# Performance work log

Measured on AMD Instinct MI355X. Metric: run time of the kernel, lower is better.

Reference implementation:

```python
import jax, jax.numpy as jnp
import numpy as np

STATE_DIM = 512
MAX_STEPS = 16
BATCH = 4096
NOISE_SCALE = 0.1


def setup_inputs() -> dict:
    key = jax.random.key(0)
    ks = jax.random.split(key, 12)
    D = STATE_DIM
    init = lambda k, shape, scale: (jax.random.normal(k, shape, dtype=jnp.float32) * scale)
    inp = {
        'initial_state': init(ks[0], (BATCH, D), 1.0),
        'noise': init(ks[1], (MAX_STEPS, BATCH, D), 1.0),
        # initial_v_proj: Linear(D, D)
        'Wv': init(ks[2], (D, D), 0.02), 'bv': jnp.zeros((D,), jnp.float32),
        # evidence_transform: Linear(2D, D) -> tanh -> Linear(D, D)
        'W1': init(ks[3], (D, 2 * D), 0.02), 'b1': jnp.zeros((D,), jnp.float32),
        'W2': init(ks[4], (D, D), 0.02), 'b2': jnp.zeros((D,), jnp.float32),
        # noise_gate: Linear(1,32) -> ReLU -> Linear(32,1) -> Sigmoid
        'Wg1': init(ks[5], (32, 1), 0.5), 'bg1': jnp.zeros((32,), jnp.float32),
        'Wg2': init(ks[6], (1, 32), 0.5), 'bg2': jnp.zeros((1,), jnp.float32),
        # clamped scalar params
        'raw_decay': jnp.float32(0.9),
        'raw_dt': jnp.float32(0.1),
        'raw_spring': jnp.float32(0.5),
        'raw_threshold': jnp.float32(0.05),
    }
    return inp


def reference(initial_state, noise, Wv, bv, W1, b1, W2, b2, Wg1, bg1, Wg2, bg2,
              raw_decay, raw_dt, raw_spring, raw_threshold):
    decay = jnp.clip(raw_decay, 0.5, 0.99)
    dt = jnp.clip(raw_dt, 0.01, 0.5)
    spring = jnp.abs(raw_spring) + 0.01
    threshold = jnp.abs(raw_threshold) + 0.0001

    x0 = initial_state
    v0 = initial_state @ Wv.T + bv  # initial_v_proj

    def step(carry, noise_t):
        x, v = carry
        gz = jnp.linalg.norm(v, axis=-1, keepdims=True)  # (B,1)
        # hopfield is None -> retrieved = zeros_like(x)
        evidence_in = jnp.concatenate([x, jnp.zeros_like(x)], axis=-1)  # (B,2D)
        force = spring * (jnp.tanh(evidence_in @ W1.T + b1) @ W2.T + b2)
        gate = jax.nn.sigmoid(jax.nn.relu(gz @ Wg1.T + bg1) @ Wg2.T + bg2)  # (B,1)
        v_new = decay * v + force + noise_t * gate * NOISE_SCALE
        x_new = x + dt * v_new
        return (x_new, v_new), (x_new, v_new, jnp.mean(gz[:, 0]))

    (xf, vf), (xs, vs, gzs) = jax.lax.scan(step, (x0, v0), noise)
    positions = jnp.concatenate([x0[None], xs], axis=0)    # (17, B, D)
    velocities = jnp.concatenate([v0[None], vs], axis=0)   # (17, B, D)
    gray_zones = jnp.concatenate(
        [jnp.mean(jnp.linalg.norm(v0, axis=-1))[None], gzs], axis=0)  # (17,)
    converged = jnp.linalg.norm(vf, axis=-1) < jax.lax.stop_gradient(threshold)
    return xf, vf, positions, velocities, gray_zones, converged
```

## Files before the change

kernel.cpp:

```cpp
#include <hip/hip_runtime.h>
#include <hip/hip_bf16.h>

#define DIM      512
#define NSTEPS   16

#define OFF_XF   0
#define OFF_VF   2097152
#define OFF_POS  4194304
#define OFF_VEL  39845888
#define OFF_GZ   75497472
#define OFF_CONV 75497489
#define SLAB     2097152

#define WS_WV 0
#define WS_W1 524288
#define WS_W2 1048576
#define WS_GZ 1572864

typedef __attribute__((ext_vector_type(8))) short short8v;
typedef __attribute__((ext_vector_type(4))) float f32x4;

__device__ __forceinline__ unsigned short f2bf(float f) {
  union { float f; unsigned u; } a; a.f = f;
  return (unsigned short)((a.u + 0x7FFFu + ((a.u >> 16) & 1u)) >> 16);
}

__device__ __forceinline__ float tanh_fast(float x) {
  float e = __expf(2.0f * x);
  return 1.0f - 2.0f / (e + 1.0f);
}

__device__ __forceinline__ void st_bf(unsigned short* lds, int r, int c, float f) {
  int byte = (c << 1) ^ ((r & 7) << 4);
  *(unsigned short*)((char*)lds + (r << 10) + byte) = f2bf(f);
}

__global__ void prep_kernel(const float* __restrict__ Wv,
                            const float* __restrict__ W1,
                            const float* __restrict__ W2,
                            unsigned short* __restrict__ ws) {
  int t = blockIdx.x * 256 + threadIdx.x;
  if (t < 32) ((float*)(ws + WS_GZ / 2))[t] = 0.0f;
  int lane = t & 63, kt = (t >> 6) & 15, nt = (t >> 10) & 31, mat = t >> 15;
  const float* W = (mat == 0) ? Wv : (mat == 1) ? W1 : W2;
  int stride = (mat == 1) ? 1024 : 512;
  unsigned short* o = ws + (mat == 0 ? WS_WV / 2 : mat == 1 ? WS_W1 / 2 : WS_W2 / 2);
  int row = nt * 16 + (lane & 15);
  int col = kt * 32 + (lane >> 4) * 8;
  const float* src = W + row * stride + col;
  short8v v;
#pragma unroll
  for (int j = 0; j < 8; ++j) v[j] = (short)f2bf(src[j]);
  *(short8v*)(o + (((nt * 16 + kt) * 64 + lane) * 8)) = v;
}

#define GEMM_512(WB) do {                                                     \
    const short8v* __wv = (const short8v*)(WB);                               \
    _Pragma("unroll")                                                         \
    for (int nt_ = 0; nt_ < 8; ++nt_) acc[nt_] = (f32x4){0.f, 0.f, 0.f, 0.f};\
    _Pragma("unroll 2")                                                       \
    for (int kt_ = 0; kt_ < 16; ++kt_) {                                      \
      short8v a_ = *(const short8v*)(aptr + ((kt_ * 64 + acol0) ^ aswz));     \
      short8v b_[8];                                                          \
      _Pragma("unroll")                                                       \
      for (int nt_ = 0; nt_ < 8; ++nt_)                                       \
        b_[nt_] = __wv[((ng8 + nt_) * 16 + kt_) * 64 + lane];                 \
      _Pragma("unroll")                                                       \
      for (int nt_ = 0; nt_ < 8; ++nt_)                                       \
        acc[nt_] = __builtin_amdgcn_mfma_f32_16x16x32_bf16(a_, b_[nt_],       \
                                                           acc[nt_], 0, 0, 0);\
    }                                                                         \
  } while (0)

__launch_bounds__(512)
__global__ void main_kernel(const float* __restrict__ x0,
                            const float* __restrict__ noise,
                            const float* __restrict__ bv,
                            const float* __restrict__ b1,
                            const float* __restrict__ b2,
                            const float* __restrict__ Wg1,
                            const float* __restrict__ bg1,
                            const float* __restrict__ Wg2,
                            const float* __restrict__ bg2,
                            const float* __restrict__ rdecay,
                            const float* __restrict__ rdt,
                            const float* __restrict__ rspring,
                            const float* __restrict__ rthr,
                            const unsigned short* __restrict__ ws,
                            float* __restrict__ gzsum,
                            float* __restrict__ out) {
  __shared__ unsigned short a_lds[32 * 512];
  __shared__ float gz_p[32];
  __shared__ float gate_lds[32];

  const int tid  = threadIdx.x;
  const int lane = tid & 63;
  const int w    = tid >> 6;
  const int mt   = w & 1;
  const int ng   = w >> 1;
  const int ng8  = ng * 8;
  const int lg   = lane >> 4;
  const int li   = lane & 15;
  const int base = blockIdx.x * 32;

  const float decay  = fminf(fmaxf(rdecay[0], 0.5f), 0.99f);
  const float dt     = fminf(fmaxf(rdt[0], 0.01f), 0.5f);
  const float spring = fabsf(rspring[0]) + 0.01f;

  const char* aptr = (const char*)a_lds + (mt * 16 + li) * 1024;
  const int acol0 = lg * 16;
  const int aswz  = (li & 7) << 4;

  int colv[8], rowv[4], rg[4];
  float b1c[8], b2c[8], bvc[8];
#pragma unroll
  for (int nt = 0; nt < 8; ++nt) {
    colv[nt] = ng * 128 + nt * 16 + li;
    b1c[nt] = b1[colv[nt]]; b2c[nt] = b2[colv[nt]]; bvc[nt] = bv[colv[nt]];
  }
#pragma unroll
  for (int j = 0; j < 4; ++j) { rowv[j] = mt * 16 + lg * 4 + j; rg[j] = (base + rowv[j]) * DIM; }

  for (int i = tid; i < 32 * DIM; i += 512) {
    int r = i >> 9, c = i & 511;
    st_bf(a_lds, r, c, x0[(base + r) * DIM + c]);
  }
  float x[8][4], v[8][4];
#pragma unroll
  for (int nt = 0; nt < 8; ++nt)
#pragma unroll
    for (int j = 0; j < 4; ++j) x[nt][j] = x0[rg[j] + colv[nt]];
  __syncthreads();

  f32x4 acc[8];
  GEMM_512(ws + WS_WV / 2);
#pragma unroll
  for (int nt = 0; nt < 8; ++nt)
#pragma unroll
    for (int j = 0; j < 4; ++j) {
      v[nt][j] = acc[nt][j] + bvc[nt];
      out[OFF_VEL + rg[j] + colv[nt]] = v[nt][j];
    }

  for (int t = 0; t < NSTEPS; ++t) {
    __syncthreads();
    if (tid < 32) gz_p[tid] = 0.0f;
    if (t > 0) {
#pragma unroll
      for (int nt = 0; nt < 8; ++nt)
#pragma unroll
        for (int j = 0; j < 4; ++j) st_bf(a_lds, rowv[j], colv[nt], x[nt][j]);
    }
    __syncthreads();

#pragma unroll
    for (int j = 0; j < 4; ++j) {
      float s = 0.f;
#pragma unroll
      for (int nt = 0; nt < 8; ++nt) s += v[nt][j] * v[nt][j];
      s += __shfl_xor(s, 1); s += __shfl_xor(s, 2);
      s += __shfl_xor(s, 4); s += __shfl_xor(s, 8);
      if (li == 0) atomicAdd(&gz_p[rowv[j]], s);
    }
    __syncthreads();

    if (tid < 32) {
      float g = sqrtf(gz_p[tid]);
      float z = bg2[0];
#pragma unroll
      for (int k = 0; k < 32; ++k) {
        float a = fmaxf(fmaf(g, Wg1[k], bg1[k]), 0.0f);
        z = fmaf(Wg2[k], a, z);
      }
      gate_lds[tid] = 1.0f / (1.0f + __expf(-z));
      float bs = g;
      bs += __shfl_xor(bs, 1); bs += __shfl_xor(bs, 2); bs += __shfl_xor(bs, 4);
      bs += __shfl_xor(bs, 8); bs += __shfl_xor(bs, 16);
      if (tid == 0) {
        atomicAdd(&gzsum[t + 1], bs);
        if (t == 0) atomicAdd(&gzsum[0], bs);
      }
    }

    GEMM_512(ws + WS_W1 / 2);
    __syncthreads();
#pragma unroll
    for (int nt = 0; nt < 8; ++nt)
#pragma unroll
      for (int j = 0; j < 4; ++j)
        st_bf(a_lds, rowv[j], colv[nt], tanh_fast(acc[nt][j] + b1c[nt]));
    __syncthreads();

    float nz[8][4];
    const float* np = noise + (size_t)t * (4096 * DIM);
#pragma unroll
    for (int nt = 0; nt < 8; ++nt)
#pragma unroll
      for (int j = 0; j < 4; ++j) nz[nt][j] = np[rg[j] + colv[nt]];

    GEMM_512(ws + WS_W2 / 2);

    float* pos = out + OFF_POS + (size_t)(t + 1) * SLAB;
    float* vel = out + OFF_VEL + (size_t)(t + 1) * SLAB;
#pragma unroll
    for (int j = 0; j < 4; ++j) {
      float g = gate_lds[rowv[j]];
#pragma unroll
      for (int nt = 0; nt < 8; ++nt) {
        float force = spring * (acc[nt][j] + b2c[nt]);
        float vn = fmaf(decay, v[nt][j], force) + nz[nt][j] * g * 0.1f;
        v[nt][j] = vn;
        x[nt][j] = fmaf(dt, vn, x[nt][j]);
        int gi = rg[j] + colv[nt];
        pos[gi] = x[nt][j];
        vel[gi] = vn;
        if (t == NSTEPS - 1) { out[OFF_XF + gi] = x[nt][j]; out[OFF_VF + gi] = vn; }
      }
    }
  }

  if (tid < 32) gz_p[tid] = 0.0f;
  __syncthreads();
#pragma unroll
  for (int j = 0; j < 4; ++j) {
    float s = 0.f;
#pragma unroll
    for (int nt = 0; nt < 8; ++nt) s += v[nt][j] * v[nt][j];
    s += __shfl_xor(s, 1); s += __shfl_xor(s, 2);
    s += __shfl_xor(s, 4); s += __shfl_xor(s, 8);
    if (li == 0) atomicAdd(&gz_p[rowv[j]], s);
  }
  __syncthreads();
  if (tid < 32) {
    float thr = fabsf(rthr[0]) + 1e-4f;
    out[OFF_CONV + base + tid] = (sqrtf(gz_p[tid]) < thr) ? 1.0f : 0.0f;
  }
}

__global__ void finalize_kernel(const float* __restrict__ gzsum,
                                float* __restrict__ out) {
  int t = threadIdx.x;
  if (t < 17) out[OFF_GZ + t] = gzsum[t] * (1.0f / 4096.0f);
}

extern "C" void kernel_launch(void* const* d_in, const int* in_sizes, int n_in,
                              void* d_out, int out_size, void* d_ws, size_t ws_size,
                              hipStream_t stream) {
  const float* x0     = (const float*)d_in[0];
  const float* noise  = (const float*)d_in[1];
  const float* Wv     = (const float*)d_in[2];
  const float* bv     = (const float*)d_in[3];
  const float* W1     = (const float*)d_in[4];
  const float* b1     = (const float*)d_in[5];
  const float* W2     = (const float*)d_in[6];
  const float* b2     = (const float*)d_in[7];
  const float* Wg1    = (const float*)d_in[8];
  const float* bg1    = (const float*)d_in[9];
  const float* Wg2    = (const float*)d_in[10];
  const float* bg2    = (const float*)d_in[11];
  const float* rdec   = (const float*)d_in[12];
  const float* rdt    = (const float*)d_in[13];
  const float* rspr   = (const float*)d_in[14];
  const float* rthr   = (const float*)d_in[15];
  unsigned short* ws  = (unsigned short*)d_ws;
  float* gz           = (float*)((char*)d_ws + WS_GZ);
  float* out          = (float*)d_out;

  hipMemcpyAsync(out + OFF_POS, x0, (size_t)4096 * DIM * sizeof(float),
                 hipMemcpyDeviceToDevice, stream);
  prep_kernel<<<384, 256, 0, stream>>>(Wv, W1, W2, ws);
  main_kernel<<<128, 512, 0, stream>>>(x0, noise, bv, b1, b2, Wg1, bg1, Wg2, bg2,
                                       rdec, rdt, rspr, rthr, ws, gz, out);
  finalize_kernel<<<1, 32, 0, stream>>>(gz, out);
}
```

Before: 675.7 us.

## Split batch into 16-row blocks with 16 waves each, software-pipelined MFMA loads

Blocks now cover 16 rows instead of 32, launched as 256 blocks of 1024 threads, so all 256 CUs get work instead of half of them. Each wave computes a 16x32 output slice. The GEMM loop prefetches the next A and B fragments one k-step ahead. The step also drops one barrier, loads noise earlier, spreads the gate MLP across a full wave, and folds the x0-to-positions copy into the kernel in place of a separate memcpy. In exchange, each block reads the full weight matrices for only 16 rows, so weight traffic through L2 doubles, and the 1024-thread blocks limit registers per thread.

```diff
diff --git a/kernel.cpp b/kernel.cpp
--- a/kernel.cpp
+++ b/kernel.cpp
@@ -3,6 +3,7 @@
 
 #define DIM      512
 #define NSTEPS   16
+#define BATCH    4096
 
 #define OFF_XF   0
 #define OFF_VF   2097152
@@ -54,25 +55,26 @@
   *(short8v*)(o + (((nt * 16 + kt) * 64 + lane) * 8)) = v;
 }
 
-#define GEMM_512(WB) do {                                                     \
-    const short8v* __wv = (const short8v*)(WB);                               \
+#define LDA(kt)     (*(const short8v*)(aptr + ((((kt) * 64) + acol0) ^ aswz)))
+#define LDB(nt, kt) (wv[(((nt) * 16 + (kt)) * 64) + lane])
+
+#define GEMM_512(WBASE) do {                                                  \
+    const short8v* wv = (const short8v*)(WBASE) + (w * 2048);                 \
+    acc[0] = (f32x4){0.f, 0.f, 0.f, 0.f};                                     \
+    acc[1] = (f32x4){0.f, 0.f, 0.f, 0.f};                                     \
+    short8v aC = LDA(0), b0 = LDB(0, 0), b1 = LDB(1, 0);                      \
     _Pragma("unroll")                                                         \
-    for (int nt_ = 0; nt_ < 8; ++nt_) acc[nt_] = (f32x4){0.f, 0.f, 0.f, 0.f};\
-    _Pragma("unroll 2")                                                       \
     for (int kt_ = 0; kt_ < 16; ++kt_) {                                      \
-      short8v a_ = *(const short8v*)(aptr + ((kt_ * 64 + acol0) ^ aswz));     \
-      short8v b_[8];                                                          \
-      _Pragma("unroll")                                                       \
-      for (int nt_ = 0; nt_ < 8; ++nt_)                                       \
-        b_[nt_] = __wv[((ng8 + nt_) * 16 + kt_) * 64 + lane];                 \
-      _Pragma("unroll")                                                       \
-      for (int nt_ = 0; nt_ < 8; ++nt_)                                       \
-        acc[nt_] = __builtin_amdgcn_mfma_f32_16x16x32_bf16(a_, b_[nt_],       \
-                                                           acc[nt_], 0, 0, 0);\
+      short8v aN = aC, b0n = b0, b1n = b1;                                    \
+      if (kt_ < 15) { aN = LDA(kt_ + 1); b0n = LDB(0, kt_ + 1);               \
+                      b1n = LDB(1, kt_ + 1); }                                \
+      acc[0] = __builtin_amdgcn_mfma_f32_16x16x32_bf16(aC, b0, acc[0],0,0,0); \
+      acc[1] = __builtin_amdgcn_mfma_f32_16x16x32_bf16(aC, b1, acc[1],0,0,0); \
+      aC = aN; b0 = b0n; b1 = b1n;                                            \
     }                                                                         \
   } while (0)
 
-__launch_bounds__(512)
+__launch_bounds__(1024, 4)
 __global__ void main_kernel(const float* __restrict__ x0,
                             const float* __restrict__ noise,
                             const float* __restrict__ bv,
@@ -89,53 +91,54 @@
                             const unsigned short* __restrict__ ws,
                             float* __restrict__ gzsum,
                             float* __restrict__ out) {
-  __shared__ unsigned short a_lds[32 * 512];
-  __shared__ float gz_p[32];
-  __shared__ float gate_lds[32];
+  __shared__ unsigned short a_lds[16 * 512];
+  __shared__ float gz_p[16];
+  __shared__ float gate_lds[16];
 
   const int tid  = threadIdx.x;
   const int lane = tid & 63;
   const int w    = tid >> 6;
-  const int mt   = w & 1;
-  const int ng   = w >> 1;
-  const int ng8  = ng * 8;
   const int lg   = lane >> 4;
   const int li   = lane & 15;
-  const int base = blockIdx.x * 32;
+  const int base = blockIdx.x * 16;
 
   const float decay  = fminf(fmaxf(rdecay[0], 0.5f), 0.99f);
   const float dt     = fminf(fmaxf(rdt[0], 0.01f), 0.5f);
   const float spring = fabsf(rspring[0]) + 0.01f;
 
-  const char* aptr = (const char*)a_lds + (mt * 16 + li) * 1024;
+  const char* aptr = (const char*)a_lds + li * 1024;
   const int acol0 = lg * 16;
   const int aswz  = (li & 7) << 4;
 
-  int colv[8], rowv[4], rg[4];
-  float b1c[8], b2c[8], bvc[8];
-#pragma unroll
-  for (int nt = 0; nt < 8; ++nt) {
-    colv[nt] = ng * 128 + nt * 16 + li;
+  int colv[2], rowv[4], rg[4];
+  float b1c[2], b2c[2], bvc[2];
+#pragma unroll
+  for (int nt = 0; nt < 2; ++nt) {
+    colv[nt] = w * 32 + nt * 16 + li;
     b1c[nt] = b1[colv[nt]]; b2c[nt] = b2[colv[nt]]; bvc[nt] = bv[colv[nt]];
   }
 #pragma unroll
-  for (int j = 0; j < 4; ++j) { rowv[j] = mt * 16 + lg * 4 + j; rg[j] = (base + rowv[j]) * DIM; }
-
-  for (int i = tid; i < 32 * DIM; i += 512) {
-    int r = i >> 9, c = i & 511;
-    st_bf(a_lds, r, c, x0[(base + r) * DIM + c]);
-  }
-  float x[8][4], v[8][4];
-#pragma unroll
-  for (int nt = 0; nt < 8; ++nt)
+  for (int j = 0; j < 4; ++j) { rowv[j] = lg * 4 + j; rg[j] = (base + rowv[j]) * DIM; }
+
+  if (tid < 16) gz_p[tid] = 0.0f;
+  for (int i = tid; i < 16 * 128; i += 1024) {
+    int r = i >> 7, c4 = (i & 127) * 4;
+    const float4 xv = *(const float4*)&x0[(base + r) * DIM + c4];
+    st_bf(a_lds, r, c4 + 0, xv.x); st_bf(a_lds, r, c4 + 1, xv.y);
+    st_bf(a_lds, r, c4 + 2, xv.z); st_bf(a_lds, r, c4 + 3, xv.w);
+    *(float4*)&out[OFF_POS + (size_t)(base + r) * DIM + c4] = xv;
+  }
+  float x[2][4], v[2][4];
+#pragma unroll
+  for (int nt = 0; nt < 2; ++nt)
 #pragma unroll
     for (int j = 0; j < 4; ++j) x[nt][j] = x0[rg[j] + colv[nt]];
   __syncthreads();
 
-  f32x4 acc[8];
-  GEMM_512(ws + WS_WV / 2);
-#pragma unroll
-  for (int nt = 0; nt < 8; ++nt)
+  f32x4 acc[2];
+  GEMM_512((const short8v*)(ws + WS_WV / 2));
+#pragma unroll
+  for (int nt = 0; nt < 2; ++nt)
 #pragma unroll
     for (int j = 0; j < 4; ++j) {
       v[nt][j] = acc[nt][j] + bvc[nt];
@@ -144,69 +147,71 @@
 
   for (int t = 0; t < NSTEPS; ++t) {
     __syncthreads();
-    if (tid < 32) gz_p[tid] = 0.0f;
     if (t > 0) {
 #pragma unroll
-      for (int nt = 0; nt < 8; ++nt)
+      for (int nt = 0; nt < 2; ++nt)
 #pragma unroll
         for (int j = 0; j < 4; ++j) st_bf(a_lds, rowv[j], colv[nt], x[nt][j]);
     }
-    __syncthreads();
-
 #pragma unroll
     for (int j = 0; j < 4; ++j) {
       float s = 0.f;
 #pragma unroll
-      for (int nt = 0; nt < 8; ++nt) s += v[nt][j] * v[nt][j];
+      for (int nt = 0; nt < 2; ++nt) s += v[nt][j] * v[nt][j];
       s += __shfl_xor(s, 1); s += __shfl_xor(s, 2);
       s += __shfl_xor(s, 4); s += __shfl_xor(s, 8);
       if (li == 0) atomicAdd(&gz_p[rowv[j]], s);
     }
     __syncthreads();
 
-    if (tid < 32) {
-      float g = sqrtf(gz_p[tid]);
-      float z = bg2[0];
-#pragma unroll
-      for (int k = 0; k < 32; ++k) {
+    float nz[2][4];
+    {
+      const float* np = noise + (size_t)t * (BATCH * DIM);
+#pragma unroll
+      for (int nt = 0; nt < 2; ++nt)
+#pragma unroll
+        for (int j = 0; j < 4; ++j) nz[nt][j] = np[rg[j] + colv[nt]];
+    }
+    if (w == 0) {
+      int r = lane >> 2, p = lane & 3;
+      float g = sqrtf(gz_p[r]);
+      float z = 0.f;
+#pragma unroll
+      for (int kk = 0; kk < 8; ++kk) {
+        int k = p * 8 + kk;
         float a = fmaxf(fmaf(g, Wg1[k], bg1[k]), 0.0f);
         z = fmaf(Wg2[k], a, z);
       }
-      gate_lds[tid] = 1.0f / (1.0f + __expf(-z));
-      float bs = g;
-      bs += __shfl_xor(bs, 1); bs += __shfl_xor(bs, 2); bs += __shfl_xor(bs, 4);
-      bs += __shfl_xor(bs, 8); bs += __shfl_xor(bs, 16);
-      if (tid == 0) {
+      z += __shfl_xor(z, 1); z += __shfl_xor(z, 2);
+      if (p == 0) gate_lds[r] = 1.0f / (1.0f + __expf(-(z + bg2[0])));
+      float bs = (p == 0) ? g : 0.f;
+      bs += __shfl_xor(bs, 1);  bs += __shfl_xor(bs, 2);
+      bs += __shfl_xor(bs, 4);  bs += __shfl_xor(bs, 8);
+      bs += __shfl_xor(bs, 16); bs += __shfl_xor(bs, 32);
+      if (lane == 0) {
         atomicAdd(&gzsum[t + 1], bs);
         if (t == 0) atomicAdd(&gzsum[0], bs);
       }
     }
-
-    GEMM_512(ws + WS_W1 / 2);
-    __syncthreads();
-#pragma unroll
-    for (int nt = 0; nt < 8; ++nt)
+    GEMM_512((const short8v*)(ws + WS_W1 / 2));
+    __syncthreads();
+
+#pragma unroll
+    for (int nt = 0; nt < 2; ++nt)
 #pragma unroll
       for (int j = 0; j < 4; ++j)
         st_bf(a_lds, rowv[j], colv[nt], tanh_fast(acc[nt][j] + b1c[nt]));
-    __syncthreads();
-
-    float nz[8][4];
-    const float* np = noise + (size_t)t * (4096 * DIM);
-#pragma unroll
-    for (int nt = 0; nt < 8; ++nt)
-#pragma unroll
-      for (int j = 0; j < 4; ++j) nz[nt][j] = np[rg[j] + colv[nt]];
-
-    GEMM_512(ws + WS_W2 / 2);
-
+    if (tid < 16) gz_p[tid] = 0.0f;
+    __syncthreads();
+
+    GEMM_512((const short8v*)(ws + WS_W2 / 2));
     float* pos = out + OFF_POS + (size_t)(t + 1) * SLAB;
     float* vel = out + OFF_VEL + (size_t)(t + 1) * SLAB;
 #pragma unroll
     for (int j = 0; j < 4; ++j) {
       float g = gate_lds[rowv[j]];
 #pragma unroll
-      for (int nt = 0; nt < 8; ++nt) {
+      for (int nt = 0; nt < 2; ++nt) {
         float force = spring * (acc[nt][j] + b2c[nt]);
         float vn = fmaf(decay, v[nt][j], force) + nz[nt][j] * g * 0.1f;
         v[nt][j] = vn;
@@ -219,19 +224,17 @@
     }
   }
 
-  if (tid < 32) gz_p[tid] = 0.0f;
-  __syncthreads();
 #pragma unroll
   for (int j = 0; j < 4; ++j) {
     float s = 0.f;
 #pragma unroll
-    for (int nt = 0; nt < 8; ++nt) s += v[nt][j] * v[nt][j];
+    for (int nt = 0; nt < 2; ++nt) s += v[nt][j] * v[nt][j];
     s += __shfl_xor(s, 1); s += __shfl_xor(s, 2);
     s += __shfl_xor(s, 4); s += __shfl_xor(s, 8);
     if (li == 0) atomicAdd(&gz_p[rowv[j]], s);
   }
   __syncthreads();
-  if (tid < 32) {
+  if (tid < 16) {
     float thr = fabsf(rthr[0]) + 1e-4f;
     out[OFF_CONV + base + tid] = (sqrtf(gz_p[tid]) < thr) ? 1.0f : 0.0f;
   }
@@ -266,10 +269,8 @@
   float* gz           = (float*)((char*)d_ws + WS_GZ);
   float* out          = (float*)d_out;
 
-  hipMemcpyAsync(out + OFF_POS, x0, (size_t)4096 * DIM * sizeof(float),
-                 hipMemcpyDeviceToDevice, stream);
   prep_kernel<<<384, 256, 0, stream>>>(Wv, W1, W2, ws);
-  main_kernel<<<128, 512, 0, stream>>>(x0, noise, bv, b1, b2, Wg1, bg1, Wg2, bg2,
-                                       rdec, rdt, rspr, rthr, ws, gz, out);
+  main_kernel<<<256, 1024, 0, stream>>>(x0, noise, bv, b1, b2, Wg1, bg1, Wg2, bg2,
+                                        rdec, rdt, rspr, rthr, ws, gz, out);
   finalize_kernel<<<1, 32, 0, stream>>>(gz, out);
 }
```

Result: slower. 997.3 us (+47.6%).

## Double workgroup threads, software-pipeline GEMM loads, fuse x0 copy, use nontemporal stores

Applied to the files above, without the earlier changes.

Each 32-row block now runs 1024 threads (16 waves), so every wave covers 64 output columns with 4 accumulators instead of 128 with 8. The GEMM loop prefetches the next k-slice of A and B into registers while the current MFMAs issue. The separate device-to-device copy of x0 into positions is folded into the kernel's initial load, which is vectorised. Noise loads are issued earlier, before the first GEMM, and all outputs use nontemporal stores. Barriers are also reordered so the gz scratch is reset in a phase that already has a sync, which removes one barrier per step. The goal is more latency hiding and fewer launches and syncs, at the cost of more per-block synchronisation among 16 waves and register pressure under the 1024-thread launch bound.

```diff
diff --git a/kernel.cpp b/kernel.cpp
--- a/kernel.cpp
+++ b/kernel.cpp
@@ -3,6 +3,7 @@
 
 #define DIM      512
 #define NSTEPS   16
+#define BATCH    4096
 
 #define OFF_XF   0
 #define OFF_VF   2097152
@@ -54,25 +55,30 @@
   *(short8v*)(o + (((nt * 16 + kt) * 64 + lane) * 8)) = v;
 }
 
-#define GEMM_512(WB) do {                                                     \
-    const short8v* __wv = (const short8v*)(WB);                               \
+#define LDA(kt)     (*(const short8v*)(aptr + ((((kt) * 64) + acol0) ^ aswz)))
+#define LDB(nt, kt) (wv[(((nt) * 16 + (kt)) * 64) + lane])
+
+#define GEMM_512(WBASE) do {                                                  \
+    const short8v* wv = (const short8v*)(WBASE) + (ng * 4096);                \
     _Pragma("unroll")                                                         \
-    for (int nt_ = 0; nt_ < 8; ++nt_) acc[nt_] = (f32x4){0.f, 0.f, 0.f, 0.f};\
-    _Pragma("unroll 2")                                                       \
+    for (int q_ = 0; q_ < 4; ++q_) acc[q_] = (f32x4){0.f, 0.f, 0.f, 0.f};     \
+    short8v aC = LDA(0);                                                      \
+    short8v bC0 = LDB(0, 0), bC1 = LDB(1, 0), bC2 = LDB(2, 0), bC3 = LDB(3, 0);\
+    _Pragma("unroll")                                                         \
     for (int kt_ = 0; kt_ < 16; ++kt_) {                                      \
-      short8v a_ = *(const short8v*)(aptr + ((kt_ * 64 + acol0) ^ aswz));     \
-      short8v b_[8];                                                          \
-      _Pragma("unroll")                                                       \
-      for (int nt_ = 0; nt_ < 8; ++nt_)                                       \
-        b_[nt_] = __wv[((ng8 + nt_) * 16 + kt_) * 64 + lane];                 \
-      _Pragma("unroll")                                                       \
-      for (int nt_ = 0; nt_ < 8; ++nt_)                                       \
-        acc[nt_] = __builtin_amdgcn_mfma_f32_16x16x32_bf16(a_, b_[nt_],       \
-                                                           acc[nt_], 0, 0, 0);\
+      short8v aN = aC, bN0 = bC0, bN1 = bC1, bN2 = bC2, bN3 = bC3;            \
+      if (kt_ < 15) { aN = LDA(kt_ + 1); bN0 = LDB(0, kt_ + 1);               \
+                      bN1 = LDB(1, kt_ + 1); bN2 = LDB(2, kt_ + 1);           \
+                      bN3 = LDB(3, kt_ + 1); }                                \
+      acc[0] = __builtin_amdgcn_mfma_f32_16x16x32_bf16(aC, bC0, acc[0],0,0,0);\
+      acc[1] = __builtin_amdgcn_mfma_f32_16x16x32_bf16(aC, bC1, acc[1],0,0,0);\
+      acc[2] = __builtin_amdgcn_mfma_f32_16x16x32_bf16(aC, bC2, acc[2],0,0,0);\
+      acc[3] = __builtin_amdgcn_mfma_f32_16x16x32_bf16(aC, bC3, acc[3],0,0,0);\
+      aC = aN; bC0 = bN0; bC1 = bN1; bC2 = bN2; bC3 = bN3;                    \
     }                                                                         \
   } while (0)
 
-__launch_bounds__(512)
+__launch_bounds__(1024)
 __global__ void main_kernel(const float* __restrict__ x0,
                             const float* __restrict__ noise,
                             const float* __restrict__ bv,
@@ -98,7 +104,6 @@
   const int w    = tid >> 6;
   const int mt   = w & 1;
   const int ng   = w >> 1;
-  const int ng8  = ng * 8;
   const int lg   = lane >> 4;
   const int li   = lane & 15;
   const int base = blockIdx.x * 32;
@@ -111,59 +116,69 @@
   const int acol0 = lg * 16;
   const int aswz  = (li & 7) << 4;
 
-  int colv[8], rowv[4], rg[4];
-  float b1c[8], b2c[8], bvc[8];
-#pragma unroll
-  for (int nt = 0; nt < 8; ++nt) {
-    colv[nt] = ng * 128 + nt * 16 + li;
+  int colv[4], rowv[4], rg[4];
+  float b1c[4], b2c[4], bvc[4];
+#pragma unroll
+  for (int nt = 0; nt < 4; ++nt) {
+    colv[nt] = ng * 64 + nt * 16 + li;
     b1c[nt] = b1[colv[nt]]; b2c[nt] = b2[colv[nt]]; bvc[nt] = bv[colv[nt]];
   }
 #pragma unroll
   for (int j = 0; j < 4; ++j) { rowv[j] = mt * 16 + lg * 4 + j; rg[j] = (base + rowv[j]) * DIM; }
 
-  for (int i = tid; i < 32 * DIM; i += 512) {
-    int r = i >> 9, c = i & 511;
-    st_bf(a_lds, r, c, x0[(base + r) * DIM + c]);
-  }
-  float x[8][4], v[8][4];
-#pragma unroll
-  for (int nt = 0; nt < 8; ++nt)
+  if (tid < 32) gz_p[tid] = 0.0f;
+  for (int i = tid; i < 32 * 128; i += 1024) {
+    int r = i >> 7, c4 = (i & 127) * 4;
+    const f32x4 xv = *(const f32x4*)&x0[(base + r) * DIM + c4];
+    st_bf(a_lds, r, c4 + 0, xv.x); st_bf(a_lds, r, c4 + 1, xv.y);
+    st_bf(a_lds, r, c4 + 2, xv.z); st_bf(a_lds, r, c4 + 3, xv.w);
+    __builtin_nontemporal_store(xv, (f32x4*)&out[OFF_POS + (size_t)(base + r) * DIM + c4]);
+  }
+  float x[4][4], v[4][4];
+#pragma unroll
+  for (int nt = 0; nt < 4; ++nt)
 #pragma unroll
     for (int j = 0; j < 4; ++j) x[nt][j] = x0[rg[j] + colv[nt]];
   __syncthreads();
 
-  f32x4 acc[8];
-  GEMM_512(ws + WS_WV / 2);
-#pragma unroll
-  for (int nt = 0; nt < 8; ++nt)
+  f32x4 acc[4];
+  GEMM_512((const short8v*)(ws + WS_WV / 2));
+#pragma unroll
+  for (int nt = 0; nt < 4; ++nt)
 #pragma unroll
     for (int j = 0; j < 4; ++j) {
       v[nt][j] = acc[nt][j] + bvc[nt];
-      out[OFF_VEL + rg[j] + colv[nt]] = v[nt][j];
+      __builtin_nontemporal_store(v[nt][j], &out[OFF_VEL + rg[j] + colv[nt]]);
     }
 
   for (int t = 0; t < NSTEPS; ++t) {
     __syncthreads();
-    if (tid < 32) gz_p[tid] = 0.0f;
     if (t > 0) {
 #pragma unroll
-      for (int nt = 0; nt < 8; ++nt)
+      for (int nt = 0; nt < 4; ++nt)
 #pragma unroll
         for (int j = 0; j < 4; ++j) st_bf(a_lds, rowv[j], colv[nt], x[nt][j]);
     }
-    __syncthreads();
-
 #pragma unroll
     for (int j = 0; j < 4; ++j) {
       float s = 0.f;
 #pragma unroll
-      for (int nt = 0; nt < 8; ++nt) s += v[nt][j] * v[nt][j];
+      for (int nt = 0; nt < 4; ++nt) s += v[nt][j] * v[nt][j];
       s += __shfl_xor(s, 1); s += __shfl_xor(s, 2);
       s += __shfl_xor(s, 4); s += __shfl_xor(s, 8);
       if (li == 0) atomicAdd(&gz_p[rowv[j]], s);
     }
     __syncthreads();
 
+    float nz[4][4];
+    {
+      const float* np = noise + (size_t)t * (BATCH * DIM);
+#pragma unroll
+      for (int nt = 0; nt < 4; ++nt)
+#pragma unroll
+        for (int j = 0; j < 4; ++j)
+          nz[nt][j] = __builtin_nontemporal_load(&np[rg[j] + colv[nt]]);
+    }
     if (tid < 32) {
       float g = sqrtf(gz_p[tid]);
       float z = bg2[0];
@@ -181,51 +196,45 @@
         if (t == 0) atomicAdd(&gzsum[0], bs);
       }
     }
-
-    GEMM_512(ws + WS_W1 / 2);
-    __syncthreads();
-#pragma unroll
-    for (int nt = 0; nt < 8; ++nt)
+    GEMM_512((const short8v*)(ws + WS_W1 / 2));
+    __syncthreads();
+
+#pragma unroll
+    for (int nt = 0; nt < 4; ++nt)
 #pragma unroll
       for (int j = 0; j < 4; ++j)
         st_bf(a_lds, rowv[j], colv[nt], tanh_fast(acc[nt][j] + b1c[nt]));
-    __syncthreads();
-
-    float nz[8][4];
-    const float* np = noise + (size_t)t * (4096 * DIM);
-#pragma unroll
-    for (int nt = 0; nt < 8; ++nt)
-#pragma unroll
-      for (int j = 0; j < 4; ++j) nz[nt][j] = np[rg[j] + colv[nt]];
-
-    GEMM_512(ws + WS_W2 / 2);
-
+    if (tid < 32) gz_p[tid] = 0.0f;
+    __syncthreads();
+
+    GEMM_512((const short8v*)(ws + WS_W2 / 2));
     float* pos = out + OFF_POS + (size_t)(t + 1) * SLAB;
     float* vel = out + OFF_VEL + (size_t)(t + 1) * SLAB;
 #pragma unroll
     for (int j = 0; j < 4; ++j) {
       float g = gate_lds[rowv[j]];
 #pragma unroll
-      for (int nt = 0; nt < 8; ++nt) {
+      for (int nt = 0; nt < 4; ++nt) {
         float force = spring * (acc[nt][j] + b2c[nt]);
         float vn = fmaf(decay, v[nt][j], force) + nz[nt][j] * g * 0.1f;
         v[nt][j] = vn;
         x[nt][j] = fmaf(dt, vn, x[nt][j]);
         int gi = rg[j] + colv[nt];
-        pos[gi] = x[nt][j];
-        vel[gi] = vn;
-        if (t == NSTEPS - 1) { out[OFF_XF + gi] = x[nt][j]; out[OFF_VF + gi] = vn; }
+        __builtin_nontemporal_store(x[nt][j], &pos[gi]);
+        __builtin_nontemporal_store(vn, &vel[gi]);
+        if (t == NSTEPS - 1) {
+          __builtin_nontemporal_store(x[nt][j], &out[OFF_XF + gi]);
+          __builtin_nontemporal_store(vn, &out[OFF_VF + gi]);
+        }
       }
     }
   }
 
-  if (tid < 32) gz_p[tid] = 0.0f;
-  __syncthreads();
 #pragma unroll
   for (int j = 0; j < 4; ++j) {
     float s = 0.f;
 #pragma unroll
-    for (int nt = 0; nt < 8; ++nt) s += v[nt][j] * v[nt][j];
+    for (int nt = 0; nt < 4; ++nt) s += v[nt][j] * v[nt][j];
     s += __shfl_xor(s, 1); s += __shfl_xor(s, 2);
     s += __shfl_xor(s, 4); s += __shfl_xor(s, 8);
     if (li == 0) atomicAdd(&gz_p[rowv[j]], s);
@@ -266,10 +275,8 @@
   float* gz           = (float*)((char*)d_ws + WS_GZ);
   float* out          = (float*)d_out;
 
-  hipMemcpyAsync(out + OFF_POS, x0, (size_t)4096 * DIM * sizeof(float),
-                 hipMemcpyDeviceToDevice, stream);
   prep_kernel<<<384, 256, 0, stream>>>(Wv, W1, W2, ws);
-  main_kernel<<<128, 512, 0, stream>>>(x0, noise, bv, b1, b2, Wg1, bg1, Wg2, bg2,
-                                       rdec, rdt, rspr, rthr, ws, gz, out);
+  main_kernel<<<128, 1024, 0, stream>>>(x0, noise, bv, b1, b2, Wg1, bg1, Wg2, bg2,
+                                        rdec, rdt, rspr, rthr, ws, gz, out);
   finalize_kernel<<<1, 32, 0, stream>>>(gz, out);
 }
```

Result: slower. 1.943 ms (+187.5%).

## Software-pipeline GEMM B/A loads and move x state to LDS

Applied to the files above, without the earlier changes.

Rewrites the inner GEMM as a fully unrolled loop with a three-deep register prefetch of the A fragments (from LDS) and B fragments (from global), so the loads for k-tile kt+3 are in flight while the MFMAs for k-tile kt run. To make room in registers for the prefetch buffers, the x state moves to an LDS fp32 buffer, noise is read inline instead of preloaded, and bv is loaded on demand. The initial-position memcpy is folded into the kernel prologue using vectorized loads, and a few barriers and gz_p resets are merged. The risks are extra LDS traffic and capacity use, noise load latency now sitting on the step's critical path, and register pressure from the 24 prefetched B vectors.

```diff
diff --git a/kernel.cpp b/kernel.cpp
--- a/kernel.cpp
+++ b/kernel.cpp
@@ -3,6 +3,7 @@
 
 #define DIM      512
 #define NSTEPS   16
+#define BATCH    4096
 
 #define OFF_XF   0
 #define OFF_VF   2097152
@@ -54,42 +55,54 @@
   *(short8v*)(o + (((nt * 16 + kt) * 64 + lane) * 8)) = v;
 }
 
-#define GEMM_512(WB) do {                                                     \
-    const short8v* __wv = (const short8v*)(WB);                               \
-    _Pragma("unroll")                                                         \
-    for (int nt_ = 0; nt_ < 8; ++nt_) acc[nt_] = (f32x4){0.f, 0.f, 0.f, 0.f};\
-    _Pragma("unroll 2")                                                       \
-    for (int kt_ = 0; kt_ < 16; ++kt_) {                                      \
-      short8v a_ = *(const short8v*)(aptr + ((kt_ * 64 + acol0) ^ aswz));     \
-      short8v b_[8];                                                          \
-      _Pragma("unroll")                                                       \
-      for (int nt_ = 0; nt_ < 8; ++nt_)                                       \
-        b_[nt_] = __wv[((ng8 + nt_) * 16 + kt_) * 64 + lane];                 \
-      _Pragma("unroll")                                                       \
-      for (int nt_ = 0; nt_ < 8; ++nt_)                                       \
-        acc[nt_] = __builtin_amdgcn_mfma_f32_16x16x32_bf16(a_, b_[nt_],       \
-                                                           acc[nt_], 0, 0, 0);\
-    }                                                                         \
+#define LDA(kt)     (*(const short8v*)(aptr + ((((kt) * 64) + acol0) ^ aswz)))
+#define LDB(nt, kt) (wv[(((ng8 + (nt)) * 16 + (kt)) * 64) + lane])
+
+#define GEMM_512(WBASE) do {                                                   \
+    const short8v* wv = (const short8v*)(WBASE);                               \
+    _Pragma("unroll")                                                          \
+    for (int q_ = 0; q_ < 8; ++q_) acc[q_] = (f32x4){0.f, 0.f, 0.f, 0.f};      \
+    short8v a0_ = LDA(0), a1_ = LDA(1), a2_ = LDA(2);                          \
+    short8v p0_[8], p1_[8], p2_[8];                                            \
+    _Pragma("unroll") for (int n_ = 0; n_ < 8; ++n_) p0_[n_] = LDB(n_, 0);     \
+    _Pragma("unroll") for (int n_ = 0; n_ < 8; ++n_) p1_[n_] = LDB(n_, 1);     \
+    _Pragma("unroll") for (int n_ = 0; n_ < 8; ++n_) p2_[n_] = LDB(n_, 2);     \
+    _Pragma("unroll")                                                          \
+    for (int kt_ = 0; kt_ < 16; ++kt_) {                                       \
+      _Pragma("unroll")                                                        \
+      for (int n_ = 0; n_ < 8; ++n_)                                           \
+        acc[n_] = __builtin_amdgcn_mfma_f32_16x16x32_bf16(a0_, p0_[n_],        \
+                                                          acc[n_], 0, 0, 0);   \
+      a0_ = a1_; a1_ = a2_;                                                    \
+      _Pragma("unroll")                                                        \
+      for (int n_ = 0; n_ < 8; ++n_) { p0_[n_] = p1_[n_]; p1_[n_] = p2_[n_]; } \
+      if (kt_ + 3 < 16) {                                                      \
+        a2_ = LDA(kt_ + 3);                                                    \
+        _Pragma("unroll")                                                      \
+        for (int n_ = 0; n_ < 8; ++n_) p2_[n_] = LDB(n_, kt_ + 3);             \
+      }                                                                        \
+    }                                                                          \
   } while (0)
 
-__launch_bounds__(512)
-__global__ void main_kernel(const float* __restrict__ x0,
-                            const float* __restrict__ noise,
-                            const float* __restrict__ bv,
-                            const float* __restrict__ b1,
-                            const float* __restrict__ b2,
-                            const float* __restrict__ Wg1,
-                            const float* __restrict__ bg1,
-                            const float* __restrict__ Wg2,
-                            const float* __restrict__ bg2,
-                            const float* __restrict__ rdecay,
-                            const float* __restrict__ rdt,
-                            const float* __restrict__ rspring,
-                            const float* __restrict__ rthr,
-                            const unsigned short* __restrict__ ws,
-                            float* __restrict__ gzsum,
-                            float* __restrict__ out) {
+__global__ __launch_bounds__(512, 1)
+void main_kernel(const float* __restrict__ x0,
+                 const float* __restrict__ noise,
+                 const float* __restrict__ bv,
+                 const float* __restrict__ b1,
+                 const float* __restrict__ b2,
+                 const float* __restrict__ Wg1,
+                 const float* __restrict__ bg1,
+                 const float* __restrict__ Wg2,
+                 const float* __restrict__ bg2,
+                 const float* __restrict__ rdecay,
+                 const float* __restrict__ rdt,
+                 const float* __restrict__ rspring,
+                 const float* __restrict__ rthr,
+                 const unsigned short* __restrict__ ws,
+                 float* __restrict__ gzsum,
+                 float* __restrict__ out) {
   __shared__ unsigned short a_lds[32 * 512];
+  __shared__ float x_lds[32 * 512];
   __shared__ float gz_p[32];
   __shared__ float gate_lds[32];
 
@@ -112,47 +125,48 @@
   const int aswz  = (li & 7) << 4;
 
   int colv[8], rowv[4], rg[4];
-  float b1c[8], b2c[8], bvc[8];
+  float b1c[8], b2c[8];
 #pragma unroll
   for (int nt = 0; nt < 8; ++nt) {
     colv[nt] = ng * 128 + nt * 16 + li;
-    b1c[nt] = b1[colv[nt]]; b2c[nt] = b2[colv[nt]]; bvc[nt] = bv[colv[nt]];
+    b1c[nt] = b1[colv[nt]]; b2c[nt] = b2[colv[nt]];
   }
 #pragma unroll
   for (int j = 0; j < 4; ++j) { rowv[j] = mt * 16 + lg * 4 + j; rg[j] = (base + rowv[j]) * DIM; }
 
-  for (int i = tid; i < 32 * DIM; i += 512) {
-    int r = i >> 9, c = i & 511;
-    st_bf(a_lds, r, c, x0[(base + r) * DIM + c]);
-  }
-  float x[8][4], v[8][4];
-#pragma unroll
-  for (int nt = 0; nt < 8; ++nt)
-#pragma unroll
-    for (int j = 0; j < 4; ++j) x[nt][j] = x0[rg[j] + colv[nt]];
+  if (tid < 32) gz_p[tid] = 0.0f;
+  for (int i = tid; i < 32 * 128; i += 512) {
+    int r = i >> 7, c4 = (i & 127) * 4;
+    const f32x4 xv = *(const f32x4*)&x0[(base + r) * DIM + c4];
+    st_bf(a_lds, r, c4 + 0, xv.x); st_bf(a_lds, r, c4 + 1, xv.y);
+    st_bf(a_lds, r, c4 + 2, xv.z); st_bf(a_lds, r, c4 + 3, xv.w);
+    *(f32x4*)&x_lds[r * 512 + c4] = xv;
+    *(f32x4*)&out[OFF_POS + (size_t)(base + r) * DIM + c4] = xv;
+  }
+  float v[8][4];
   __syncthreads();
 
   f32x4 acc[8];
   GEMM_512(ws + WS_WV / 2);
 #pragma unroll
-  for (int nt = 0; nt < 8; ++nt)
+  for (int nt = 0; nt < 8; ++nt) {
+    float bvc = bv[colv[nt]];
 #pragma unroll
     for (int j = 0; j < 4; ++j) {
-      v[nt][j] = acc[nt][j] + bvc[nt];
+      v[nt][j] = acc[nt][j] + bvc;
       out[OFF_VEL + rg[j] + colv[nt]] = v[nt][j];
     }
+  }
 
   for (int t = 0; t < NSTEPS; ++t) {
     __syncthreads();
-    if (tid < 32) gz_p[tid] = 0.0f;
     if (t > 0) {
 #pragma unroll
       for (int nt = 0; nt < 8; ++nt)
 #pragma unroll
-        for (int j = 0; j < 4; ++j) st_bf(a_lds, rowv[j], colv[nt], x[nt][j]);
-    }
-    __syncthreads();
-
+        for (int j = 0; j < 4; ++j)
+          st_bf(a_lds, rowv[j], colv[nt], x_lds[rowv[j] * 512 + colv[nt]]);
+    }
 #pragma unroll
     for (int j = 0; j < 4; ++j) {
       float s = 0.f;
@@ -184,43 +198,38 @@
 
     GEMM_512(ws + WS_W1 / 2);
     __syncthreads();
+
 #pragma unroll
     for (int nt = 0; nt < 8; ++nt)
 #pragma unroll
       for (int j = 0; j < 4; ++j)
         st_bf(a_lds, rowv[j], colv[nt], tanh_fast(acc[nt][j] + b1c[nt]));
-    __syncthreads();
-
-    float nz[8][4];
-    const float* np = noise + (size_t)t * (4096 * DIM);
-#pragma unroll
-    for (int nt = 0; nt < 8; ++nt)
-#pragma unroll
-      for (int j = 0; j < 4; ++j) nz[nt][j] = np[rg[j] + colv[nt]];
+    if (tid < 32) gz_p[tid] = 0.0f;
+    __syncthreads();
 
     GEMM_512(ws + WS_W2 / 2);
 
     float* pos = out + OFF_POS + (size_t)(t + 1) * SLAB;
     float* vel = out + OFF_VEL + (size_t)(t + 1) * SLAB;
+    const float* np = noise + (size_t)t * (BATCH * DIM);
 #pragma unroll
     for (int j = 0; j < 4; ++j) {
       float g = gate_lds[rowv[j]];
 #pragma unroll
       for (int nt = 0; nt < 8; ++nt) {
         float force = spring * (acc[nt][j] + b2c[nt]);
-        float vn = fmaf(decay, v[nt][j], force) + nz[nt][j] * g * 0.1f;
+        float vn = fmaf(decay, v[nt][j], force) + np[rg[j] + colv[nt]] * g * 0.1f;
         v[nt][j] = vn;
-        x[nt][j] = fmaf(dt, vn, x[nt][j]);
+        float xn = fmaf(dt, vn, x_lds[rowv[j] * 512 + colv[nt]]);
+        x_lds[rowv[j] * 512 + colv[nt]] = xn;
         int gi = rg[j] + colv[nt];
-        pos[gi] = x[nt][j];
+        pos[gi] = xn;
         vel[gi] = vn;
-        if (t == NSTEPS - 1) { out[OFF_XF + gi] = x[nt][j]; out[OFF_VF + gi] = vn; }
+        if (t == NSTEPS - 1) { out[OFF_XF + gi] = xn; out[OFF_VF + gi] = vn; }
       }
     }
   }
 
-  if (tid < 32) gz_p[tid] = 0.0f;
-  __syncthreads();
 #pragma unroll
   for (int j = 0; j < 4; ++j) {
     float s = 0.f;
@@ -266,8 +275,6 @@
   float* gz           = (float*)((char*)d_ws + WS_GZ);
   float* out          = (float*)d_out;
 
-  hipMemcpyAsync(out + OFF_POS, x0, (size_t)4096 * DIM * sizeof(float),
-                 hipMemcpyDeviceToDevice, stream);
   prep_kernel<<<384, 256, 0, stream>>>(Wv, W1, W2, ws);
   main_kernel<<<128, 512, 0, stream>>>(x0, noise, bv, b1, b2, Wg1, bg1, Wg2, bg2,
                                        rdec, rdt, rspr, rthr, ws, gz, out);
```

Measured after the change: 2.245 ms. 3.32x slower.
